# Kernel tuning notes

Hardware: AMD Instinct MI355X
Metric: run time of the kernel (lower is better)

The kernel has to match this reference:

```python
import jax, jax.numpy as jnp
import numpy as np
import math

EMBED_DIM = 1024
NUM_HEADS = 16
HEAD_DIM = EMBED_DIM // NUM_HEADS
MAX_POSITION = 1024
BATCH = 4
SEQ_LEN = 1024


def setup_inputs() -> dict:
    key = jax.random.key(0)
    ks = jax.random.split(key, 10)
    s = 1.0 / math.sqrt(EMBED_DIM)
    inp = {
        "x": jax.random.normal(ks[0], (BATCH, SEQ_LEN, EMBED_DIM), dtype=jnp.float32),
        "Wq": jax.random.normal(ks[1], (EMBED_DIM, EMBED_DIM), dtype=jnp.float32) * s,
        "bq": jnp.zeros((EMBED_DIM,), dtype=jnp.float32),
        "Wk": jax.random.normal(ks[2], (EMBED_DIM, EMBED_DIM), dtype=jnp.float32) * s,
        "bk": jnp.zeros((EMBED_DIM,), dtype=jnp.float32),
        "Wv": jax.random.normal(ks[3], (EMBED_DIM, EMBED_DIM), dtype=jnp.float32) * s,
        "bv": jnp.zeros((EMBED_DIM,), dtype=jnp.float32),
        "Wo": jax.random.normal(ks[4], (EMBED_DIM, EMBED_DIM), dtype=jnp.float32) * s,
        "bo": jnp.zeros((EMBED_DIM,), dtype=jnp.float32),
        "rel_key": jax.random.normal(ks[5], (MAX_POSITION, HEAD_DIM), dtype=jnp.float32),
    }
    return inp


def reference(x, Wq, bq, Wk, bk, Wv, bv, Wo, bo, rel_key):
    B, S, E = x.shape
    H, D = NUM_HEADS, HEAD_DIM
    # projections, split heads -> (B, H, S, D)
    Q = (x @ Wq + bq).reshape(B, S, H, D).transpose(0, 2, 1, 3)
    K = (x @ Wk + bk).reshape(B, S, H, D).transpose(0, 2, 1, 3)
    V = (x @ Wv + bv).reshape(B, S, H, D).transpose(0, 2, 1, 3)
    # content scores
    attn_content = jnp.einsum('bhqd,bhkd->bhqk', Q, K)
    # relative-position scores via skew trick
    rel = rel_key[MAX_POSITION - S:, :]              # (S, D)
    QEr = jnp.einsum('bhqd,sd->bhqs', Q, rel)        # (B, H, S, S)
    padded = jnp.pad(QEr, ((0, 0), (0, 0), (0, 0), (1, 0)))  # (B, H, S, S+1)
    Srel = padded.reshape(B, H, S + 1, S)[:, :, 1:, :]       # (B, H, S, S)
    scores = (attn_content + Srel) * (1.0 / math.sqrt(D))
    # causal mask
    mask = jnp.tril(jnp.ones((S, S), dtype=bool))
    scores = jnp.where(mask[None, None], scores, -jnp.inf)
    w = jax.nn.softmax(scores, axis=-1)
    out = jnp.einsum('bhqk,bhkd->bhqd', w, V)
    out = out.transpose(0, 2, 1, 3).reshape(B, S, E)
    return out @ Wo + bo
```

## Files before the change

### kernel.cpp

```cpp
#include <hip/hip_runtime.h>

typedef unsigned short u16;
typedef __attribute__((ext_vector_type(8))) __bf16 bf16x8;
typedef __attribute__((ext_vector_type(4))) float f32x4;
typedef __attribute__((ext_vector_type(4))) u16 u16x4;


__device__ __forceinline__ u16 f2bf(float f) {
  unsigned u = __float_as_uint(f);
  u += 0x7fff + ((u >> 16) & 1);
  return (u16)(u >> 16);
}

__device__ __forceinline__ f32x4 mfma16(bf16x8 a, bf16x8 b, f32x4 c) {
  return __builtin_amdgcn_mfma_f32_16x16x32_bf16(a, b, c, 0, 0, 0);
}

__device__ __forceinline__ void gload16(const void* g, void* l) {
  __builtin_amdgcn_global_load_lds(
      (__attribute__((address_space(1))) unsigned int*)(const_cast<void*>(g)),
      (__attribute__((address_space(3))) unsigned int*)l, 16, 0, 0);
}


__global__ void k_prep_all(const float* __restrict__ x, u16* __restrict__ xb,
                           const float* __restrict__ W0, const float* __restrict__ W1,
                           const float* __restrict__ W2, const float* __restrict__ W3,
                           u16* __restrict__ Wt,
                           const float* __restrict__ rel, u16* __restrict__ relb,
                           const float* __restrict__ bq, const float* __restrict__ bk,
                           const float* __restrict__ bv, float* __restrict__ bias) {
  __shared__ float tile[32][33];
  const int bx = blockIdx.x, t = threadIdx.x;
  if (bx < 4096) {
    int i = bx * 256 + t;
    float4 v = reinterpret_cast<const float4*>(x)[i];
    u16x4 o;
    o.x = f2bf(v.x); o.y = f2bf(v.y); o.z = f2bf(v.z); o.w = f2bf(v.w);
    reinterpret_cast<u16x4*>(xb)[i] = o;
  } else if (bx < 8192) {
    const int id = bx - 4096;
    const int z = id >> 10;
    const float* in = (z == 0) ? W0 : (z == 1) ? W1 : (z == 2) ? W2 : W3;
    u16* out = Wt + (size_t)z * 1024 * 1024;
    const int r0 = ((id >> 5) & 31) * 32, c0 = (id & 31) * 32;
    for (int i = t; i < 1024; i += 256) {
      int r = i >> 5, c = i & 31;
      tile[r][c] = in[(size_t)(r0 + r) * 1024 + c0 + c];
    }
    __syncthreads();
    for (int i = t; i < 1024; i += 256) {
      int r = i >> 5, c = i & 31;
      out[(size_t)(c0 + r) * 1024 + r0 + c] = f2bf(tile[c][r]);
    }
  } else if (bx < 8256) {
    int i = (bx - 8192) * 256 + t;
    float4 v = reinterpret_cast<const float4*>(rel)[i];
    u16x4 o;
    o.x = f2bf(v.x); o.y = f2bf(v.y); o.z = f2bf(v.z); o.w = f2bf(v.w);
    reinterpret_cast<u16x4*>(relb)[i] = o;
  } else {
    int i = (bx - 8256) * 256 + t;
    if (i < 3072) bias[i] = (i < 1024) ? bq[i] : (i < 2048 ? bk[i - 1024] : bv[i - 2048]);
  }
}


template<int MODE, int BN>
__global__ __launch_bounds__(256) void k_gemm(
    const u16* __restrict__ A, const u16* __restrict__ B,
    const float* __restrict__ bias, void* __restrict__ Cout,
    u16* __restrict__ Vaux, int M, int N, int Kd)
{
  constexpr int NF = BN / 32;
  __shared__ u16 Alds[128 * 64];
  __shared__ u16 Blds[BN * 64];
  const int t = threadIdx.x;
  const int lane = t & 63, wid = t >> 6;
  const int wr = wid >> 1, wc = wid & 1;
  const int l15 = lane & 15, lg = lane >> 4;
  const int m0 = blockIdx.y * 128, n0 = blockIdx.x * BN;

  const f32x4 fzero = {0.f, 0.f, 0.f, 0.f};
  f32x4 acc[4][NF];
#pragma unroll
  for (int i = 0; i < 4; i++)
#pragma unroll
    for (int j = 0; j < NF; j++) acc[i][j] = fzero;

  const int srow = t >> 3;
  const int scb  = ((t & 7) * 16) ^ ((srow & 7) << 4);
  const size_t abase = (size_t)(m0 + srow) * Kd + (scb >> 1);
  const size_t bbase = (size_t)(n0 + srow) * Kd + (scb >> 1);

  for (int k0 = 0; k0 < Kd; k0 += 64) {
#pragma unroll
    for (int ci = 0; ci < 4; ci++)
      gload16(A + abase + (size_t)(32 * ci) * Kd + k0, Alds + (t + 256 * ci) * 8);
#pragma unroll
    for (int ci = 0; ci < NF; ci++)
      gload16(B + bbase + (size_t)(32 * ci) * Kd + k0, Blds + (t + 256 * ci) * 8);
    __syncthreads();
#pragma unroll
    for (int kk = 0; kk < 2; kk++) {
      bf16x8 av[4], bv[NF];
#pragma unroll
      for (int mi = 0; mi < 4; mi++) {
        const int row = wr * 64 + mi * 16 + l15;
        av[mi] = *reinterpret_cast<const bf16x8*>(
            (const char*)Alds + row * 128 + ((kk * 64 + lg * 16) ^ ((row & 7) << 4)));
      }
#pragma unroll
      for (int ni = 0; ni < NF; ni++) {
        const int row = wc * (BN / 2) + ni * 16 + l15;
        bv[ni] = *reinterpret_cast<const bf16x8*>(
            (const char*)Blds + row * 128 + ((kk * 64 + lg * 16) ^ ((row & 7) << 4)));
      }
#pragma unroll
      for (int mi = 0; mi < 4; mi++)
#pragma unroll
        for (int ni = 0; ni < NF; ni++)
          acc[mi][ni] = mfma16(av[mi], bv[ni], acc[mi][ni]);
    }
    __syncthreads();
  }

#pragma unroll
  for (int mi = 0; mi < 4; mi++) {
#pragma unroll
    for (int ni = 0; ni < NF; ni++) {
      const int col = n0 + wc * (BN / 2) + ni * 16 + l15;
      const float bcol = bias[col];
#pragma unroll
      for (int r = 0; r < 4; r++) {
        const int row = m0 + wr * 64 + mi * 16 + lg * 4 + r;
        const float v = acc[mi][ni][r] + bcol;
        if (MODE == 0) {
          ((float*)Cout)[(size_t)row * N + col] = v;
        } else {
          if (col < 2048) {
            ((u16*)Cout)[(size_t)row * N + col] = f2bf(v);
          } else {
            const int bb = row >> 10, ss = row & 1023;
            Vaux[((size_t)bb * 1024 + (col - 2048)) * 1024 + ss] = f2bf(v);
          }
        }
      }
    }
  }
}


__global__ __launch_bounds__(256, 4) void k_attn(
    const u16* __restrict__ qkv,
    const u16* __restrict__ vt,
    const u16* __restrict__ relb,
    u16* __restrict__ Oout)
{
  __shared__ u16 Klds[64 * 64];
  __shared__ u16 Vlds[64 * 64];
  __shared__ float Sbuf[4][16 * 84];

  const int t = threadIdx.x;
  const int lane = t & 63, w = t >> 6;
  const int l15 = lane & 15, lg = lane >> 4;
  const int blk = blockIdx.x;
  const int bh = blk & 63;
  const int g = blk >> 6;
  const int jq = g >> 2, rq = g & 3;
  const int qbt = (jq == 0) ? (15 - rq) : (jq == 1) ? (8 + rq) : (jq == 2) ? (7 - rq) : rq;
  const int b = bh >> 4, h = bh & 15;
  const int qb = qbt * 64;
  const int qw = qb + w * 16;

  float* Wb = Sbuf[w];
  u16* Pb = (u16*)Sbuf[w];

  const f32x4 fzero = {0.f, 0.f, 0.f, 0.f};

  const size_t qrow = (size_t)(b * 1024 + qw + l15) * 3072 + h * 64;
  bf16x8 aQ0 = *reinterpret_cast<const bf16x8*>(qkv + qrow + lg * 8);
  bf16x8 aQ1 = *reinterpret_cast<const bf16x8*>(qkv + qrow + 32 + lg * 8);

  f32x4 oacc[4];
  float l_r[4];
#pragma unroll
  for (int r = 0; r < 4; r++) { oacc[r] = fzero; l_r[r] = 0.f; }

  const int srow = t >> 3;
  const int scb = ((t & 7) * 16) ^ ((srow & 7) << 4);
  const u16* Ks0 = qkv + (size_t)(b * 1024 + srow) * 3072 + 1024 + h * 64 + (scb >> 1);
  const u16* Ks1 = Ks0 + 32 * 3072;
  const u16* Vs0 = vt + (size_t)(bh * 64 + srow) * 1024 + (scb >> 1);
  const u16* Vs1 = Vs0 + 32 * 1024;
  u16* Kd0 = Klds + t * 8;  u16* Kd1 = Klds + (t + 256) * 8;
  u16* Vd0 = Vlds + t * 8;  u16* Vd1 = Vlds + (t + 256) * 8;

  const int nk = qbt + 1;
  const float SC = 0.125f * 1.44269504f;

  for (int kt = 0; kt < nk; kt++) {
    const int k0 = kt * 64;
    gload16(Ks0 + (size_t)k0 * 3072, Kd0);
    gload16(Ks1 + (size_t)k0 * 3072, Kd1);
    gload16(Vs0 + k0, Vd0);
    gload16(Vs1 + k0, Vd1);
    __syncthreads();

    __builtin_amdgcn_s_setprio(1);
    f32x4 sc4[4];
#pragma unroll
    for (int tt = 0; tt < 4; tt++) sc4[tt] = fzero;
#pragma unroll
    for (int tt = 0; tt < 4; tt++) {
      const int row = tt * 16 + l15;
      const int sw = (row & 7) << 4;
      bf16x8 b0 = *reinterpret_cast<const bf16x8*>((const char*)Klds + row * 128 + ((lg * 16) ^ sw));
      bf16x8 b1 = *reinterpret_cast<const bf16x8*>((const char*)Klds + row * 128 + ((64 + lg * 16) ^ sw));
      sc4[tt] = mfma16(aQ0, b0, sc4[tt]);
      sc4[tt] = mfma16(aQ1, b1, sc4[tt]);
    }

    const int rbase = 1008 + k0 - qw;
#pragma unroll
    for (int wj = 0; wj < 5; wj++) {
      int rr = rbase + wj * 16 + l15;
      rr = rr < 0 ? 0 : (rr > 1023 ? 1023 : rr);
      const u16* rp = relb + rr * 64;
      bf16x8 b0 = *reinterpret_cast<const bf16x8*>(rp + lg * 8);
      bf16x8 b1 = *reinterpret_cast<const bf16x8*>(rp + 32 + lg * 8);
      f32x4 z = fzero;
      z = mfma16(aQ0, b0, z);
      z = mfma16(aQ1, b1, z);
#pragma unroll
      for (int r = 0; r < 4; r++)
        Wb[(lg * 4 + r) * 84 + wj * 16 + l15] = z[r];
    }
    __builtin_amdgcn_s_setprio(0);
    __builtin_amdgcn_wave_barrier();

    float pvv[4][4];
#pragma unroll
    for (int r = 0; r < 4; r++) {
      const int rowi = lg * 4 + r;
      const int q = qw + rowi;
      const float* wrow = Wb + rowi * 84 + (15 - rowi);
#pragma unroll
      for (int tt = 0; tt < 4; tt++) {
        const int kg = k0 + tt * 16 + l15;
        float s = (sc4[tt][r] + wrow[tt * 16 + l15]) * SC;
        s = (kg <= q) ? s : -1e30f;
        float p = exp2f(s);
        pvv[tt][r] = p;
        l_r[r] += p;
      }
    }
    __builtin_amdgcn_wave_barrier();
    asm volatile("" ::: "memory");

#pragma unroll
    for (int tt = 0; tt < 4; tt++)
#pragma unroll
      for (int r = 0; r < 4; r++) {
        const int rowi = lg * 4 + r;
        const int cb = (32 * tt + 2 * l15) ^ ((rowi & 7) << 4);
        *(u16*)((char*)Pb + rowi * 128 + cb) = f2bf(pvv[tt][r]);
      }
    __builtin_amdgcn_wave_barrier();

    __builtin_amdgcn_s_setprio(1);
#pragma unroll
    for (int s = 0; s < 2; s++) {
      const int acb = (s * 64 + lg * 16) ^ ((l15 & 7) << 4);
      bf16x8 aP = *reinterpret_cast<const bf16x8*>((const char*)Pb + l15 * 128 + acb);
#pragma unroll
      for (int dt = 0; dt < 4; dt++) {
        const int vrow = dt * 16 + l15;
        const int vcb = (s * 64 + lg * 16) ^ ((vrow & 7) << 4);
        bf16x8 bV = *reinterpret_cast<const bf16x8*>((const char*)Vlds + vrow * 128 + vcb);
        oacc[dt] = mfma16(aP, bV, oacc[dt]);
      }
    }
    __builtin_amdgcn_s_setprio(0);
    __syncthreads();
  }

#pragma unroll
  for (int r = 0; r < 4; r++) {
    float l = l_r[r];
#pragma unroll
    for (int xm = 1; xm < 16; xm <<= 1) l += __shfl_xor(l, xm);
    const float inv = 1.f / l;
    const int q = qw + lg * 4 + r;
#pragma unroll
    for (int dt = 0; dt < 4; dt++)
      Oout[(size_t)(b * 1024 + q) * 1024 + h * 64 + dt * 16 + l15] = f2bf(oacc[dt][r] * inv);
  }
}


extern "C" void kernel_launch(void* const* d_in, const int* in_sizes, int n_in,
                              void* d_out, int out_size, void* d_ws, size_t ws_size,
                              hipStream_t stream) {
  const float* x   = (const float*)d_in[0];
  const float* Wq  = (const float*)d_in[1];
  const float* bq  = (const float*)d_in[2];
  const float* Wk  = (const float*)d_in[3];
  const float* bk  = (const float*)d_in[4];
  const float* Wv  = (const float*)d_in[5];
  const float* bv  = (const float*)d_in[6];
  const float* Wo  = (const float*)d_in[7];
  const float* bo  = (const float*)d_in[8];
  const float* rel = (const float*)d_in[9];

  const size_t MB = 1024 * 1024;
  char* ws = (char*)d_ws;
  u16*   xb    = (u16*)(ws);
  u16*   Wt    = (u16*)(ws + 8 * MB);
  u16*   qkvb  = (u16*)(ws + 16 * MB);
  u16*   vtb   = (u16*)(ws + 40 * MB);
  u16*   relbb = (u16*)(ws + 48 * MB);
  float* bqkv  = (float*)(ws + 49 * MB);
  u16*   Ob    = xb;

  k_prep_all<<<8268, 256, 0, stream>>>(x, xb, Wq, Wk, Wv, Wo, Wt, rel, relbb, bq, bk, bv, bqkv);

  k_gemm<2, 128><<<dim3(24, 32), 256, 0, stream>>>(xb, Wt, bqkv, qkvb, vtb, 4096, 3072, 1024);

  k_attn<<<1024, 256, 0, stream>>>(qkvb, vtb, relbb, Ob);

  k_gemm<0, 64><<<dim3(16, 32), 256, 0, stream>>>(Ob, Wt + 3 * MB, bo, d_out, nullptr, 4096, 1024, 1024);
}
```

Measured before the change: 128.3 us.

## Double-buffer output-projection GEMM and vectorize weight transpose loads/stores

Adds an optional double-buffered LDS pipeline to the GEMM kernel, so the next K tile's global-to-LDS loads are issued before computing on the current tile. It is enabled only for the output projection GEMM and uses one barrier per iteration instead of two. The weight transpose in the prep kernel now uses float4 loads and 4-wide bf16 stores instead of scalar accesses. The double buffer doubles LDS use for that GEMM, and the lone barrier may not fully guarantee that the async loads have landed before they are read.

```diff
diff --git a/kernel.cpp b/kernel.cpp
--- a/kernel.cpp
+++ b/kernel.cpp
@@ -44,15 +44,19 @@
     const float* in = (z == 0) ? W0 : (z == 1) ? W1 : (z == 2) ? W2 : W3;
     u16* out = Wt + (size_t)z * 1024 * 1024;
     const int r0 = ((id >> 5) & 31) * 32, c0 = (id & 31) * 32;
-    for (int i = t; i < 1024; i += 256) {
-      int r = i >> 5, c = i & 31;
-      tile[r][c] = in[(size_t)(r0 + r) * 1024 + c0 + c];
-    }
+    const int r = t >> 3, c4 = t & 7;
+    float4 v = *reinterpret_cast<const float4*>(&in[(size_t)(r0 + r) * 1024 + c0 + c4 * 4]);
+    tile[r][c4 * 4 + 0] = v.x;
+    tile[r][c4 * 4 + 1] = v.y;
+    tile[r][c4 * 4 + 2] = v.z;
+    tile[r][c4 * 4 + 3] = v.w;
     __syncthreads();
-    for (int i = t; i < 1024; i += 256) {
-      int r = i >> 5, c = i & 31;
-      out[(size_t)(c0 + r) * 1024 + r0 + c] = f2bf(tile[c][r]);
-    }
+    u16x4 o;
+    o.x = f2bf(tile[c4 * 4 + 0][r]);
+    o.y = f2bf(tile[c4 * 4 + 1][r]);
+    o.z = f2bf(tile[c4 * 4 + 2][r]);
+    o.w = f2bf(tile[c4 * 4 + 3][r]);
+    *reinterpret_cast<u16x4*>(&out[(size_t)(c0 + r) * 1024 + r0 + c4 * 4]) = o;
   } else if (bx < 8256) {
     int i = (bx - 8192) * 256 + t;
     float4 v = reinterpret_cast<const float4*>(rel)[i];
@@ -66,15 +70,16 @@
 }
 
 
-template<int MODE, int BN>
+template<int MODE, int BN, int PIPE>
 __global__ __launch_bounds__(256) void k_gemm(
     const u16* __restrict__ A, const u16* __restrict__ B,
     const float* __restrict__ bias, void* __restrict__ Cout,
     u16* __restrict__ Vaux, int M, int N, int Kd)
 {
   constexpr int NF = BN / 32;
-  __shared__ u16 Alds[128 * 64];
-  __shared__ u16 Blds[BN * 64];
+  constexpr int NB = PIPE ? 2 : 1;
+  __shared__ u16 Alds[NB][128 * 64];
+  __shared__ u16 Blds[NB][BN * 64];
   const int t = threadIdx.x;
   const int lane = t & 63, wid = t >> 6;
   const int wr = wid >> 1, wc = wid & 1;
@@ -93,14 +98,16 @@
   const size_t abase = (size_t)(m0 + srow) * Kd + (scb >> 1);
   const size_t bbase = (size_t)(n0 + srow) * Kd + (scb >> 1);
 
-  for (int k0 = 0; k0 < Kd; k0 += 64) {
+  auto stage = [&](int buf, int k0) {
 #pragma unroll
     for (int ci = 0; ci < 4; ci++)
-      gload16(A + abase + (size_t)(32 * ci) * Kd + k0, Alds + (t + 256 * ci) * 8);
+      gload16(A + abase + (size_t)(32 * ci) * Kd + k0, Alds[buf] + (t + 256 * ci) * 8);
 #pragma unroll
     for (int ci = 0; ci < NF; ci++)
-      gload16(B + bbase + (size_t)(32 * ci) * Kd + k0, Blds + (t + 256 * ci) * 8);
-    __syncthreads();
+      gload16(B + bbase + (size_t)(32 * ci) * Kd + k0, Blds[buf] + (t + 256 * ci) * 8);
+  };
+
+  auto compute = [&](int buf) {
 #pragma unroll
     for (int kk = 0; kk < 2; kk++) {
       bf16x8 av[4], bv[NF];
@@ -108,13 +115,13 @@
       for (int mi = 0; mi < 4; mi++) {
         const int row = wr * 64 + mi * 16 + l15;
         av[mi] = *reinterpret_cast<const bf16x8*>(
-            (const char*)Alds + row * 128 + ((kk * 64 + lg * 16) ^ ((row & 7) << 4)));
+            (const char*)Alds[buf] + row * 128 + ((kk * 64 + lg * 16) ^ ((row & 7) << 4)));
       }
 #pragma unroll
       for (int ni = 0; ni < NF; ni++) {
         const int row = wc * (BN / 2) + ni * 16 + l15;
         bv[ni] = *reinterpret_cast<const bf16x8*>(
-            (const char*)Blds + row * 128 + ((kk * 64 + lg * 16) ^ ((row & 7) << 4)));
+            (const char*)Blds[buf] + row * 128 + ((kk * 64 + lg * 16) ^ ((row & 7) << 4)));
       }
 #pragma unroll
       for (int mi = 0; mi < 4; mi++)
@@ -122,7 +129,24 @@
         for (int ni = 0; ni < NF; ni++)
           acc[mi][ni] = mfma16(av[mi], bv[ni], acc[mi][ni]);
     }
-    __syncthreads();
+  };
+
+  if (PIPE) {
+    stage(0, 0);
+    int cur = 0;
+    for (int k0 = 0; k0 < Kd; k0 += 64) {
+      __syncthreads();
+      if (k0 + 64 < Kd) stage(cur ^ 1, k0 + 64);
+      compute(cur);
+      cur ^= 1;
+    }
+  } else {
+    for (int k0 = 0; k0 < Kd; k0 += 64) {
+      stage(0, k0);
+      __syncthreads();
+      compute(0);
+      __syncthreads();
+    }
   }
 
 #pragma unroll
@@ -325,9 +349,9 @@
 
   k_prep_all<<<8268, 256, 0, stream>>>(x, xb, Wq, Wk, Wv, Wo, Wt, rel, relbb, bq, bk, bv, bqkv);
 
-  k_gemm<2, 128><<<dim3(24, 32), 256, 0, stream>>>(xb, Wt, bqkv, qkvb, vtb, 4096, 3072, 1024);
+  k_gemm<2, 128, 0><<<dim3(24, 32), 256, 0, stream>>>(xb, Wt, bqkv, qkvb, vtb, 4096, 3072, 1024);
 
   k_attn<<<1024, 256, 0, stream>>>(qkvb, vtb, relbb, Ob);
 
-  k_gemm<0, 64><<<dim3(16, 32), 256, 0, stream>>>(Ob, Wt + 3 * MB, bo, d_out, nullptr, 4096, 1024, 1024);
-}
+  k_gemm<0, 64, 1><<<dim3(16, 32), 256, 0, stream>>>(Ob, Wt + 3 * MB, bo, d_out, nullptr, 4096, 1024, 1024);
+}
```

Result: no change. 126.0 us (median of 3 runs) (-1.8%).
